# Kernel optimization log

Hardware: AMD Instinct MI355X
Metric: run time of the kernel (lower is better)

## Reference

```python
import jax, jax.numpy as jnp
import numpy as np

B, S, D = 8, 512, 768
HEADS = 16           # label_n
HD = 64              # size_per_head
NEG = 1e12


def setup_inputs() -> dict:
    key = jax.random.key(0)
    k1, k2, k3 = jax.random.split(key, 3)
    hidden = jax.random.normal(k1, (B, S, D), dtype=jnp.float32)
    token_ids = jax.random.randint(k2, (B, S), 0, 21128, dtype=jnp.int32)
    W = jax.random.normal(k3, (D, HEADS * 2 * HD), dtype=jnp.float32) * 0.02
    b = jnp.zeros((HEADS * 2 * HD,), dtype=jnp.float32)
    return {"hidden": hidden, "token_ids": token_ids, "W": W, "b": b}


def _rope(x):
    # x: [B, S, H, HD] -> RoPE-rotated, Su Jianlin interleaved convention
    d = x.shape[-1]
    inv_freq = 1.0 / (10000.0 ** (jnp.arange(0, d, 2, dtype=jnp.float32) / d))  # [d/2]
    pos = jnp.arange(x.shape[1], dtype=jnp.float32)                              # [S]
    freqs = pos[:, None] * inv_freq[None, :]                                     # [S, d/2]
    sin = jnp.repeat(jnp.sin(freqs), 2, axis=-1)[None, :, None, :]               # [1,S,1,d]
    cos = jnp.repeat(jnp.cos(freqs), 2, axis=-1)[None, :, None, :]
    x2 = jnp.stack([-x[..., 1::2], x[..., 0::2]], axis=-1).reshape(x.shape)
    return x * cos + x2 * sin


def reference(hidden, token_ids, W, b):
    # qk projection: [B,S,H,2,HD]
    qk = (hidden @ W + b).reshape(B, S, HEADS, 2, HD)
    q, k = qk[..., 0, :], qk[..., 1, :]          # [B,S,H,HD]
    q = _rope(q)
    k = _rope(k)
    # all-pairs span scores per entity head
    logits = jnp.einsum('bmhd,bnhd->bhmn', q, k) / jnp.sqrt(jnp.float32(HD))
    # padding mask from token ids (0 = pad)
    mask = (token_ids > 0).astype(logits.dtype)  # [B,S]
    logits = logits - (1.0 - mask[:, None, :, None]) * NEG
    logits = logits - (1.0 - mask[:, None, None, :]) * NEG
    # strict lower-triangular mask (spans must have start <= end)
    tril = jnp.tril(jnp.ones((S, S), dtype=logits.dtype), k=-1)
    logits = logits - tril[None, None, :, :] * NEG
    # valid-span weight mask (upper triangle incl. diag, both positions valid)
    tri_mask = (1.0 - tril)[None, None, :, :] * mask[:, None, :, None] * mask[:, None, None, :]
    return logits, tri_mask
```

## Files before the change

### kernel.cpp

```cpp
#include <hip/hip_runtime.h>
#include <hip/hip_bf16.h>
#include <cstdint>
#include <cstddef>


#define NEGV 1.0e12f

typedef short bf16x8 __attribute__((ext_vector_type(8)));
typedef float f32x4  __attribute__((ext_vector_type(4)));

static __device__ __forceinline__ short f2b(float x) {
    __hip_bfloat16 h = __float2bfloat16(x);
    union { __hip_bfloat16 h; short s; } u; u.h = h; return u.s;
}
static __device__ __forceinline__ float b2f(short s) {
    union { short s; __hip_bfloat16 h; } u; u.s = s; return __bfloat162float(u.h);
}

__global__ __launch_bounds__(256) void cast_kernel(const float* __restrict__ hidden,
                                                   const float* __restrict__ W,
                                                   short* __restrict__ Xb,
                                                   short* __restrict__ Wt) {
    const int E1 = 4096 * 768;
    const int E2 = 768 * 2048;
    int i = blockIdx.x * 256 + threadIdx.x;
    if (i < E1) {
        Xb[i] = f2b(hidden[i]);
    } else if (i < E1 + E2) {
        int j = i - E1;
        int n = j / 768, k = j - n * 768;
        Wt[j] = f2b(W[k * 2048 + n]);
    }
}

__global__ __launch_bounds__(256) void gemm_qk(const short* __restrict__ A,
                                               const short* __restrict__ Bt,
                                               const float* __restrict__ bias,
                                               short* __restrict__ C) {
    __shared__ short As[128 * 32];
    __shared__ short Bs[128 * 32];
    const int m0 = (blockIdx.x >> 4) * 128;
    const int n0 = (blockIdx.x & 15) * 128;
    const int tid  = threadIdx.x;
    const int wave = tid >> 6, lane = tid & 63;
    const int quad = lane >> 4, r16 = lane & 15;
    const int wm = (wave >> 1) * 64, wn = (wave & 1) * 64;

    const int srow = tid >> 2;
    const int scol = (tid & 3) * 8;
    const short* Ap0 = A  + (m0 + srow) * 768 + scol;
    const short* Ap1 = A  + (m0 + 64 + srow) * 768 + scol;
    const short* Bp0 = Bt + (n0 + srow) * 768 + scol;
    const short* Bp1 = Bt + (n0 + 64 + srow) * 768 + scol;
    short* As0 = As + srow * 32 + scol;
    short* As1 = As + (64 + srow) * 32 + scol;
    short* Bs0 = Bs + srow * 32 + scol;
    short* Bs1 = Bs + (64 + srow) * 32 + scol;

    f32x4 acc[4][4] = {};

    for (int k0 = 0; k0 < 768; k0 += 32) {
        __syncthreads();
        *(bf16x8*)As0 = *(const bf16x8*)(Ap0 + k0);
        *(bf16x8*)As1 = *(const bf16x8*)(Ap1 + k0);
        *(bf16x8*)Bs0 = *(const bf16x8*)(Bp0 + k0);
        *(bf16x8*)Bs1 = *(const bf16x8*)(Bp1 + k0);
        __syncthreads();

        bf16x8 af[4], bfr[4];
#pragma unroll
        for (int mi = 0; mi < 4; ++mi)
            af[mi] = *(const bf16x8*)(As + (wm + mi * 16 + r16) * 32 + quad * 8);
#pragma unroll
        for (int ni = 0; ni < 4; ++ni)
            bfr[ni] = *(const bf16x8*)(Bs + (wn + ni * 16 + r16) * 32 + quad * 8);
#pragma unroll
        for (int mi = 0; mi < 4; ++mi)
#pragma unroll
            for (int ni = 0; ni < 4; ++ni)
                acc[mi][ni] = __builtin_amdgcn_mfma_f32_16x16x32_bf16(
                    af[mi], bfr[ni], acc[mi][ni], 0, 0, 0);
    }

#pragma unroll
    for (int mi = 0; mi < 4; ++mi)
#pragma unroll
        for (int ni = 0; ni < 4; ++ni) {
            int col = n0 + wn + ni * 16 + r16;
            float bv = bias[col];
            int rowb = m0 + wm + mi * 16 + quad * 4;
#pragma unroll
            for (int r = 0; r < 4; ++r)
                C[(rowb + r) * 2048 + col] = f2b(acc[mi][ni][r] + bv);
        }
}

__global__ __launch_bounds__(256) void rope_kernel(const short* __restrict__ QK,
                                                   short* __restrict__ Q,
                                                   short* __restrict__ K) {
    int t = blockIdx.x * 256 + threadIdx.x;
    int i = t & 31;
    int rr = t >> 5;
    int which = rr & 1; rr >>= 1;
    int h = rr & 15;    rr >>= 4;
    int s = rr & 511;
    int b = rr >> 9;

    int src = (b * 512 + s) * 2048 + h * 128 + which * 64 + 2 * i;
    float f0 = b2f(QK[src]), f1 = b2f(QK[src + 1]);

    float ang = (float)s * exp2f(-0.4152410118609203f * (float)i);
    float sn, cs;
    __sincosf(ang, &sn, &cs);
    float o0 = f0 * cs - f1 * sn;
    float o1 = f1 * cs + f0 * sn;

    short* dst = (which ? K : Q) + ((b * 16 + h) * 512 + s) * 64 + 2 * i;
    dst[0] = f2b(o0);
    dst[1] = f2b(o1);
}

__global__ __launch_bounds__(256) void logits_kernel(const short* __restrict__ Q,
                                                     const short* __restrict__ K,
                                                     const int* __restrict__ tok,
                                                     float* __restrict__ out) {
    __shared__ short Qs[128 * 64];
    __shared__ short Ks[128 * 64];
    __shared__ float rowNeg[128];
    __shared__ float colNeg[128];

    int blk = blockIdx.x;
    int nt = blk & 3, mt = (blk >> 2) & 3, bh = blk >> 4;
    int b = bh >> 4;
    int m0 = mt * 128, n0 = nt * 128;

    const int tid  = threadIdx.x;
    const int wave = tid >> 6, lane = tid & 63;
    const int quad = lane >> 4, r16 = lane & 15;
    const int wm = (wave >> 1) * 64, wn = (wave & 1) * 64;

    const short* Qbase = Q + (bh * 512 + m0) * 64;
    const short* Kbase = K + (bh * 512 + n0) * 64;
#pragma unroll
    for (int p = 0; p < 4; ++p) {
        int e = p * 2048 + tid * 8;
        *(bf16x8*)(Qs + e) = *(const bf16x8*)(Qbase + e);
        *(bf16x8*)(Ks + e) = *(const bf16x8*)(Kbase + e);
    }
    if (tid < 128)        rowNeg[tid]        = (tok[b * 512 + m0 + tid] > 0) ? 0.f : NEGV;
    else if (tid < 256)   colNeg[tid - 128]  = (tok[b * 512 + n0 + (tid - 128)] > 0) ? 0.f : NEGV;
    __syncthreads();

    f32x4 acc[4][4] = {};
#pragma unroll
    for (int kk = 0; kk < 64; kk += 32) {
        bf16x8 af[4], bfr[4];
#pragma unroll
        for (int mi = 0; mi < 4; ++mi)
            af[mi] = *(const bf16x8*)(Qs + (wm + mi * 16 + r16) * 64 + kk + quad * 8);
#pragma unroll
        for (int ni = 0; ni < 4; ++ni)
            bfr[ni] = *(const bf16x8*)(Ks + (wn + ni * 16 + r16) * 64 + kk + quad * 8);
#pragma unroll
        for (int mi = 0; mi < 4; ++mi)
#pragma unroll
            for (int ni = 0; ni < 4; ++ni)
                acc[mi][ni] = __builtin_amdgcn_mfma_f32_16x16x32_bf16(
                    af[mi], bfr[ni], acc[mi][ni], 0, 0, 0);
    }

    float* obase = out + (size_t)bh * 512 * 512;
#pragma unroll
    for (int mi = 0; mi < 4; ++mi)
#pragma unroll
        for (int ni = 0; ni < 4; ++ni) {
            int n = n0 + wn + ni * 16 + r16;
            float cn = colNeg[n - n0];
#pragma unroll
            for (int r = 0; r < 4; ++r) {
                int m = m0 + wm + mi * 16 + quad * 4 + r;
                float v = acc[mi][ni][r] * 0.125f - rowNeg[m - m0] - cn
                          - ((m > n) ? NEGV : 0.0f);
                obase[(size_t)m * 512 + n] = v;
            }
        }
}

__global__ __launch_bounds__(256) void trimask_kernel(const int* __restrict__ tok,
                                                      float* __restrict__ out2) {
    int t = blockIdx.x * 256 + threadIdx.x;
    int n4 = (t & 127) << 2;
    int rr = t >> 7;
    int m = rr & 511;
    int b = rr >> 9;
    float mm = (tok[b * 512 + m] > 0) ? 1.0f : 0.0f;
    f32x4 v;
#pragma unroll
    for (int j = 0; j < 4; ++j) {
        int n = n4 + j;
        float mn = (tok[b * 512 + n] > 0) ? 1.0f : 0.0f;
        v[j] = (m > n) ? 0.0f : (mm * mn);
    }
    *(f32x4*)(out2 + (size_t)(b * 512 + m) * 512 + n4) = v;
}

extern "C" void kernel_launch(void* const* d_in, const int* in_sizes, int n_in,
                              void* d_out, int out_size, void* d_ws, size_t ws_size,
                              hipStream_t stream) {
    const float* hidden = (const float*)d_in[0];
    const int*   tok    = (const int*)d_in[1];
    const float* W      = (const float*)d_in[2];
    const float* bias   = (const float*)d_in[3];
    float* out  = (float*)d_out;
    float* out2 = out + 33554432;

    char* ws = (char*)d_ws;
    short* QKi = (short*)(ws);
    short* Xb  = (short*)(ws + 16777216);
    short* Wt  = (short*)(ws + 23068672);
    short* Qb  = (short*)(ws + 16777216);
    short* Kb  = (short*)(ws + 25165824);

    hipLaunchKernelGGL(cast_kernel,    dim3(18432), dim3(256), 0, stream, hidden, W, Xb, Wt);
    hipLaunchKernelGGL(gemm_qk,        dim3(512),   dim3(256), 0, stream, Xb, Wt, bias, QKi);
    hipLaunchKernelGGL(rope_kernel,    dim3(16384), dim3(256), 0, stream, QKi, Qb, Kb);
    hipLaunchKernelGGL(logits_kernel,  dim3(2048),  dim3(256), 0, stream, Qb, Kb, tok, out);
    hipLaunchKernelGGL(trimask_kernel, dim3(2048),  dim3(256), 0, stream, tok, out2);
}
```

Before: 210.2 us.

## Fuse RoPE and tri-mask into logits kernel, vectorize casts, use LDS-direct loads

Splits the cast into a vectorized hidden cast that also builds sin/cos tables, plus a tiled LDS transpose for W. The GEMM now uses global_load_lds for its tile staging. RoPE is applied while the logits kernel loads Q/K from the projection output, which removes the separate rope pass and its Q/K round trip through memory. The tri-mask output is written by the h==0 logits blocks, removing a kernel launch. In exchange the logits prologue does more work, the tri-mask writes land unevenly on those blocks, and the global_load_lds lane-to-LDS mapping has to match the tile layout exactly.

```diff
diff --git a/kernel.cpp b/kernel.cpp
--- a/kernel.cpp
+++ b/kernel.cpp
@@ -17,20 +17,65 @@
     union { short s; __hip_bfloat16 h; } u; u.s = s; return __bfloat162float(u.h);
 }
 
-__global__ __launch_bounds__(256) void cast_kernel(const float* __restrict__ hidden,
-                                                   const float* __restrict__ W,
+static __device__ __forceinline__ void gload16(const short* g, short* l) {
+    __builtin_amdgcn_global_load_lds(
+        (const __attribute__((address_space(1))) void*)g,
+        (__attribute__((address_space(3))) void*)l, 16, 0, 0);
+}
+
+__global__ __launch_bounds__(256) void prep_kernel(const float* __restrict__ hidden,
                                                    short* __restrict__ Xb,
+                                                   float* __restrict__ SinT,
+                                                   float* __restrict__ CosT) {
+    int t = blockIdx.x * 256 + threadIdx.x;
+    if (t < 393216) {
+        const float4* hp = (const float4*)hidden;
+        float4 a = hp[t * 2];
+        float4 c = hp[t * 2 + 1];
+        bf16x8 v;
+        v[0] = f2b(a.x); v[1] = f2b(a.y); v[2] = f2b(a.z); v[3] = f2b(a.w);
+        v[4] = f2b(c.x); v[5] = f2b(c.y); v[6] = f2b(c.z); v[7] = f2b(c.w);
+        *(bf16x8*)(Xb + t * 8) = v;
+    } else if (t < 393216 + 16384) {
+        int u = t - 393216;
+        int s = u >> 5, i = u & 31;
+        float ang = (float)s * exp2f(-0.4152410118609203f * (float)i);
+        float sn, cs;
+        __sincosf(ang, &sn, &cs);
+        SinT[u] = sn;
+        CosT[u] = cs;
+    }
+}
+
+__global__ __launch_bounds__(256) void transpose_w(const float* __restrict__ W,
                                                    short* __restrict__ Wt) {
-    const int E1 = 4096 * 768;
-    const int E2 = 768 * 2048;
-    int i = blockIdx.x * 256 + threadIdx.x;
-    if (i < E1) {
-        Xb[i] = f2b(hidden[i]);
-    } else if (i < E1 + E2) {
-        int j = i - E1;
-        int n = j / 768, k = j - n * 768;
-        Wt[j] = f2b(W[k * 2048 + n]);
-    }
+    __shared__ short T[64 * 68];
+    int k0 = (blockIdx.x % 12) * 64;
+    int n0 = (blockIdx.x / 12) * 64;
+    int tid = threadIdx.x;
+
+    int r = tid >> 2;
+    int cbase = (tid & 3) * 4;
+#pragma unroll
+    for (int q = 0; q < 4; ++q) {
+        int c = cbase + q * 16;
+        float4 v = *(const float4*)(W + (size_t)(k0 + r) * 2048 + n0 + c);
+        short* tp = T + r * 68 + c;
+        tp[0] = f2b(v.x); tp[1] = f2b(v.y); tp[2] = f2b(v.z); tp[3] = f2b(v.w);
+    }
+    __syncthreads();
+
+    int n = tid >> 2;
+    int kc = (tid & 3) * 16;
+    bf16x8 o0, o1;
+#pragma unroll
+    for (int j = 0; j < 8; ++j) {
+        o0[j] = T[(kc + j) * 68 + n];
+        o1[j] = T[(kc + 8 + j) * 68 + n];
+    }
+    short* wp = Wt + (size_t)(n0 + n) * 768 + k0 + kc;
+    *(bf16x8*)wp       = o0;
+    *(bf16x8*)(wp + 8) = o1;
 }
 
 __global__ __launch_bounds__(256) void gemm_qk(const short* __restrict__ A,
@@ -46,25 +91,25 @@
     const int quad = lane >> 4, r16 = lane & 15;
     const int wm = (wave >> 1) * 64, wn = (wave & 1) * 64;
 
-    const int srow = tid >> 2;
-    const int scol = (tid & 3) * 8;
-    const short* Ap0 = A  + (m0 + srow) * 768 + scol;
-    const short* Ap1 = A  + (m0 + 64 + srow) * 768 + scol;
-    const short* Bp0 = Bt + (n0 + srow) * 768 + scol;
-    const short* Bp1 = Bt + (n0 + 64 + srow) * 768 + scol;
-    short* As0 = As + srow * 32 + scol;
-    short* As1 = As + (64 + srow) * 32 + scol;
-    short* Bs0 = Bs + srow * 32 + scol;
-    short* Bs1 = Bs + (64 + srow) * 32 + scol;
+    const int srow = wave * 32 + (lane >> 2);
+    const int scol = (lane & 3) * 8;
+    const short* gA0 = A  + (size_t)(m0 + srow) * 768 + scol;
+    const short* gA1 = gA0 + 16 * 768;
+    const short* gB0 = Bt + (size_t)(n0 + srow) * 768 + scol;
+    const short* gB1 = gB0 + 16 * 768;
+    short* lA0 = As + (wave * 32) * 32;
+    short* lA1 = As + (wave * 32 + 16) * 32;
+    short* lB0 = Bs + (wave * 32) * 32;
+    short* lB1 = Bs + (wave * 32 + 16) * 32;
 
     f32x4 acc[4][4] = {};
 
     for (int k0 = 0; k0 < 768; k0 += 32) {
         __syncthreads();
-        *(bf16x8*)As0 = *(const bf16x8*)(Ap0 + k0);
-        *(bf16x8*)As1 = *(const bf16x8*)(Ap1 + k0);
-        *(bf16x8*)Bs0 = *(const bf16x8*)(Bp0 + k0);
-        *(bf16x8*)Bs1 = *(const bf16x8*)(Bp1 + k0);
+        gload16(gA0 + k0, lA0);
+        gload16(gA1 + k0, lA1);
+        gload16(gB0 + k0, lB0);
+        gload16(gB1 + k0, lB1);
         __syncthreads();
 
         bf16x8 af[4], bfr[4];
@@ -91,47 +136,24 @@
             int rowb = m0 + wm + mi * 16 + quad * 4;
 #pragma unroll
             for (int r = 0; r < 4; ++r)
-                C[(rowb + r) * 2048 + col] = f2b(acc[mi][ni][r] + bv);
-        }
-}
-
-__global__ __launch_bounds__(256) void rope_kernel(const short* __restrict__ QK,
-                                                   short* __restrict__ Q,
-                                                   short* __restrict__ K) {
-    int t = blockIdx.x * 256 + threadIdx.x;
-    int i = t & 31;
-    int rr = t >> 5;
-    int which = rr & 1; rr >>= 1;
-    int h = rr & 15;    rr >>= 4;
-    int s = rr & 511;
-    int b = rr >> 9;
-
-    int src = (b * 512 + s) * 2048 + h * 128 + which * 64 + 2 * i;
-    float f0 = b2f(QK[src]), f1 = b2f(QK[src + 1]);
-
-    float ang = (float)s * exp2f(-0.4152410118609203f * (float)i);
-    float sn, cs;
-    __sincosf(ang, &sn, &cs);
-    float o0 = f0 * cs - f1 * sn;
-    float o1 = f1 * cs + f0 * sn;
-
-    short* dst = (which ? K : Q) + ((b * 16 + h) * 512 + s) * 64 + 2 * i;
-    dst[0] = f2b(o0);
-    dst[1] = f2b(o1);
-}
-
-__global__ __launch_bounds__(256) void logits_kernel(const short* __restrict__ Q,
-                                                     const short* __restrict__ K,
+                C[(size_t)(rowb + r) * 2048 + col] = f2b(acc[mi][ni][r] + bv);
+        }
+}
+
+__global__ __launch_bounds__(256) void logits_kernel(const short* __restrict__ QKi,
+                                                     const float* __restrict__ SinT,
+                                                     const float* __restrict__ CosT,
                                                      const int* __restrict__ tok,
-                                                     float* __restrict__ out) {
-    __shared__ short Qs[128 * 64];
-    __shared__ short Ks[128 * 64];
+                                                     float* __restrict__ out,
+                                                     float* __restrict__ out2) {
+    __shared__ short Qs[128 * 72];
+    __shared__ short Ks[128 * 72];
     __shared__ float rowNeg[128];
     __shared__ float colNeg[128];
 
     int blk = blockIdx.x;
     int nt = blk & 3, mt = (blk >> 2) & 3, bh = blk >> 4;
-    int b = bh >> 4;
+    int b = bh >> 4, h = bh & 15;
     int m0 = mt * 128, n0 = nt * 128;
 
     const int tid  = threadIdx.x;
@@ -139,16 +161,41 @@
     const int quad = lane >> 4, r16 = lane & 15;
     const int wm = (wave >> 1) * 64, wn = (wave & 1) * 64;
 
-    const short* Qbase = Q + (bh * 512 + m0) * 64;
-    const short* Kbase = K + (bh * 512 + n0) * 64;
-#pragma unroll
-    for (int p = 0; p < 4; ++p) {
-        int e = p * 2048 + tid * 8;
-        *(bf16x8*)(Qs + e) = *(const bf16x8*)(Qbase + e);
-        *(bf16x8*)(Ks + e) = *(const bf16x8*)(Kbase + e);
-    }
-    if (tid < 128)        rowNeg[tid]        = (tok[b * 512 + m0 + tid] > 0) ? 0.f : NEGV;
-    else if (tid < 256)   colNeg[tid - 128]  = (tok[b * 512 + n0 + (tid - 128)] > 0) ? 0.f : NEGV;
+    int row = tid >> 1;
+    int ch  = (tid & 1) * 32;
+    int sQ = m0 + row, sK = n0 + row;
+    const short* qsrc = QKi + ((size_t)(b * 512 + sQ)) * 2048 + h * 128 + ch;
+    const short* ksrc = QKi + ((size_t)(b * 512 + sK)) * 2048 + h * 128 + 64 + ch;
+    const float* sQs = SinT + sQ * 32;  const float* sQc = CosT + sQ * 32;
+    const float* sKs = SinT + sK * 32;  const float* sKc = CosT + sK * 32;
+
+#pragma unroll
+    for (int j = 0; j < 4; ++j) {
+        int i0 = (ch >> 1) + j * 4;
+        bf16x8 v = *(const bf16x8*)(qsrc + j * 8);
+        f32x4 sn = *(const f32x4*)(sQs + i0);
+        f32x4 cs = *(const f32x4*)(sQc + i0);
+        bf16x8 o;
+#pragma unroll
+        for (int p = 0; p < 4; ++p) {
+            float f0 = b2f(v[2 * p]), f1 = b2f(v[2 * p + 1]);
+            o[2 * p]     = f2b(f0 * cs[p] - f1 * sn[p]);
+            o[2 * p + 1] = f2b(f1 * cs[p] + f0 * sn[p]);
+        }
+        *(bf16x8*)(Qs + row * 72 + ch + j * 8) = o;
+        v  = *(const bf16x8*)(ksrc + j * 8);
+        sn = *(const f32x4*)(sKs + i0);
+        cs = *(const f32x4*)(sKc + i0);
+#pragma unroll
+        for (int p = 0; p < 4; ++p) {
+            float f0 = b2f(v[2 * p]), f1 = b2f(v[2 * p + 1]);
+            o[2 * p]     = f2b(f0 * cs[p] - f1 * sn[p]);
+            o[2 * p + 1] = f2b(f1 * cs[p] + f0 * sn[p]);
+        }
+        *(bf16x8*)(Ks + row * 72 + ch + j * 8) = o;
+    }
+    if (tid < 128)        rowNeg[tid]       = (tok[b * 512 + m0 + tid] > 0) ? 0.f : NEGV;
+    else if (tid < 256)   colNeg[tid - 128] = (tok[b * 512 + n0 + (tid - 128)] > 0) ? 0.f : NEGV;
     __syncthreads();
 
     f32x4 acc[4][4] = {};
@@ -157,10 +204,10 @@
         bf16x8 af[4], bfr[4];
 #pragma unroll
         for (int mi = 0; mi < 4; ++mi)
-            af[mi] = *(const bf16x8*)(Qs + (wm + mi * 16 + r16) * 64 + kk + quad * 8);
+            af[mi] = *(const bf16x8*)(Qs + (wm + mi * 16 + r16) * 72 + kk + quad * 8);
 #pragma unroll
         for (int ni = 0; ni < 4; ++ni)
-            bfr[ni] = *(const bf16x8*)(Ks + (wn + ni * 16 + r16) * 64 + kk + quad * 8);
+            bfr[ni] = *(const bf16x8*)(Ks + (wn + ni * 16 + r16) * 72 + kk + quad * 8);
 #pragma unroll
         for (int mi = 0; mi < 4; ++mi)
 #pragma unroll
@@ -184,24 +231,23 @@
                 obase[(size_t)m * 512 + n] = v;
             }
         }
-}
-
-__global__ __launch_bounds__(256) void trimask_kernel(const int* __restrict__ tok,
-                                                      float* __restrict__ out2) {
-    int t = blockIdx.x * 256 + threadIdx.x;
-    int n4 = (t & 127) << 2;
-    int rr = t >> 7;
-    int m = rr & 511;
-    int b = rr >> 9;
-    float mm = (tok[b * 512 + m] > 0) ? 1.0f : 0.0f;
-    f32x4 v;
-#pragma unroll
-    for (int j = 0; j < 4; ++j) {
-        int n = n4 + j;
-        float mn = (tok[b * 512 + n] > 0) ? 1.0f : 0.0f;
-        v[j] = (m > n) ? 0.0f : (mm * mn);
-    }
-    *(f32x4*)(out2 + (size_t)(b * 512 + m) * 512 + n4) = v;
+
+    if (h == 0) {
+        float* o2 = out2 + (size_t)b * 512 * 512;
+#pragma unroll
+        for (int mi = 0; mi < 4; ++mi)
+#pragma unroll
+            for (int ni = 0; ni < 4; ++ni) {
+                int n = n0 + wn + ni * 16 + r16;
+                float mn = (colNeg[n - n0] == 0.f) ? 1.f : 0.f;
+#pragma unroll
+                for (int r = 0; r < 4; ++r) {
+                    int m = m0 + wm + mi * 16 + quad * 4 + r;
+                    float mm = (rowNeg[m - m0] == 0.f) ? 1.f : 0.f;
+                    o2[(size_t)m * 512 + n] = (m > n) ? 0.f : (mm * mn);
+                }
+            }
+    }
 }
 
 extern "C" void kernel_launch(void* const* d_in, const int* in_sizes, int n_in,
@@ -215,15 +261,14 @@
     float* out2 = out + 33554432;
 
     char* ws = (char*)d_ws;
-    short* QKi = (short*)(ws);
-    short* Xb  = (short*)(ws + 16777216);
-    short* Wt  = (short*)(ws + 23068672);
-    short* Qb  = (short*)(ws + 16777216);
-    short* Kb  = (short*)(ws + 25165824);
-
-    hipLaunchKernelGGL(cast_kernel,    dim3(18432), dim3(256), 0, stream, hidden, W, Xb, Wt);
-    hipLaunchKernelGGL(gemm_qk,        dim3(512),   dim3(256), 0, stream, Xb, Wt, bias, QKi);
-    hipLaunchKernelGGL(rope_kernel,    dim3(16384), dim3(256), 0, stream, QKi, Qb, Kb);
-    hipLaunchKernelGGL(logits_kernel,  dim3(2048),  dim3(256), 0, stream, Qb, Kb, tok, out);
-    hipLaunchKernelGGL(trimask_kernel, dim3(2048),  dim3(256), 0, stream, tok, out2);
-}
+    short* QKi  = (short*)(ws);
+    short* Xb   = (short*)(ws + 16777216);
+    short* Wt   = (short*)(ws + 23068672);
+    float* SinT = (float*)(ws + 26214400);
+    float* CosT = (float*)(ws + 26279936);
+
+    hipLaunchKernelGGL(prep_kernel,   dim3(1600), dim3(256), 0, stream, hidden, Xb, SinT, CosT);
+    hipLaunchKernelGGL(transpose_w,   dim3(384),  dim3(256), 0, stream, W, Wt);
+    hipLaunchKernelGGL(gemm_qk,       dim3(512),  dim3(256), 0, stream, Xb, Wt, bias, QKi);
+    hipLaunchKernelGGL(logits_kernel, dim3(2048), dim3(256), 0, stream, QKi, SinT, CosT, tok, out, out2);
+}
```

After: 198.8 us. -5.4%, faster.
